# Kernel tuning notes

Measured on AMD Instinct MI355X. Metric: run time of the kernel, lower is better.

## Reference

```python
import jax, jax.numpy as jnp
import numpy as np

VOCAB = 100000
NUM_SENSES = 8
VEC_DIM = 128
BATCH = 16384
CTX = 10  # context words -> x has 2 + CTX columns


def setup_inputs() -> dict:
    key = jax.random.key(0)
    kx, kg, ks = jax.random.split(key, 3)
    x = jax.random.randint(kx, (BATCH, 2 + CTX), 0, VOCAB, dtype=jnp.int32)
    W_g = jax.random.normal(kg, (VOCAB, VEC_DIM), dtype=jnp.float32) * 0.1
    W_s = jax.random.normal(ks, (VOCAB, NUM_SENSES, VEC_DIM), dtype=jnp.float32) * 0.1
    return {"x": x, "W_g": W_g, "W_s": W_s}


def reference(x, W_g, W_s):
    # sum of global vectors of the context words: [B, D]
    sum_context = jnp.sum(W_g[x[:, 2:]], axis=1)
    # sense vectors of the target word: [B, K, D]
    sense_vecs = W_s[x[:, 0]]
    # per-sense score against the context: [B, K]
    scores = jnp.einsum("bkd,bd->bk", sense_vecs, sum_context)
    # route to best sense per example: [B]
    right_senses = jnp.argmax(scores, axis=1)
    # gather the chosen sense vector: [B, D]
    chosen = jnp.take_along_axis(sense_vecs, right_senses[:, None, None], axis=1)[:, 0, :]
    # dot with the global vector of the second word -> [B, 1], sigmoid activation
    dot_prod = jnp.einsum("bd,bd->b", chosen, W_g[x[:, 1]])[:, None]
    return jax.nn.sigmoid(dot_prod)
```

## Files before the change

### kernel.cpp

```cpp
#include <hip/hip_runtime.h>
#include <hip/hip_bf16.h>
#include <cmath>

#define BATCH     16384
#define CTX       10
#define NSENSE    8
#define VEC_DIM   128
#define XCOLS     (2 + CTX)

__global__ __launch_bounds__(256) void SenseEmbedding_40295383171457_kernel(
    const int*   __restrict__ x,
    const float* __restrict__ Wg,
    const float* __restrict__ Ws,
    float*       __restrict__ out)
{
    const int gtid = blockIdx.x * blockDim.x + threadIdx.x;
    const int elem = gtid >> 4;
    const int sub  = gtid & 15;
    if (elem >= BATCH) return;

    const int* xr = x + elem * XCOLS;
    const int w0 = xr[0];
    const int w1 = xr[1];
    const int off = sub * 8;

    float4 c0 = make_float4(0.f, 0.f, 0.f, 0.f);
    float4 c1 = make_float4(0.f, 0.f, 0.f, 0.f);
    #pragma unroll
    for (int c = 0; c < CTX; ++c) {
        const float* row = Wg + (size_t)xr[2 + c] * VEC_DIM + off;
        const float4 a = *reinterpret_cast<const float4*>(row);
        const float4 b = *reinterpret_cast<const float4*>(row + 4);
        c0.x += a.x; c0.y += a.y; c0.z += a.z; c0.w += a.w;
        c1.x += b.x; c1.y += b.y; c1.z += b.z; c1.w += b.w;
    }

    const float* srow = Ws + (size_t)w0 * (NSENSE * VEC_DIM);
    float scores[NSENSE];
    #pragma unroll
    for (int k = 0; k < NSENSE; ++k) {
        const float* r = srow + k * VEC_DIM + off;
        const float4 a = *reinterpret_cast<const float4*>(r);
        const float4 b = *reinterpret_cast<const float4*>(r + 4);
        float p = a.x * c0.x + a.y * c0.y + a.z * c0.z + a.w * c0.w
                + b.x * c1.x + b.y * c1.y + b.z * c1.z + b.w * c1.w;
        #pragma unroll
        for (int s = 8; s > 0; s >>= 1)
            p += __shfl_xor(p, s, 16);
        scores[k] = p;
    }

    int   best = 0;
    float bv   = scores[0];
    #pragma unroll
    for (int k = 1; k < NSENSE; ++k) {
        if (scores[k] > bv) { bv = scores[k]; best = k; }
    }

    const float* ch = srow + best * VEC_DIM + off;
    const float4 ca = *reinterpret_cast<const float4*>(ch);
    const float4 cb = *reinterpret_cast<const float4*>(ch + 4);
    const float* tg = Wg + (size_t)w1 * VEC_DIM + off;
    const float4 ta = *reinterpret_cast<const float4*>(tg);
    const float4 tb = *reinterpret_cast<const float4*>(tg + 4);
    float d = ca.x * ta.x + ca.y * ta.y + ca.z * ta.z + ca.w * ta.w
            + cb.x * tb.x + cb.y * tb.y + cb.z * tb.z + cb.w * tb.w;
    #pragma unroll
    for (int s = 8; s > 0; s >>= 1)
        d += __shfl_xor(d, s, 16);

    if (sub == 0) {
        out[elem] = 1.f / (1.f + expf(-d));
    }
}

extern "C" void kernel_launch(void* const* d_in, const int* in_sizes, int n_in,
                              void* d_out, int out_size, void* d_ws, size_t ws_size,
                              hipStream_t stream) {
    const int*   x  = (const int*)  d_in[0];
    const float* Wg = (const float*)d_in[1];
    const float* Ws = (const float*)d_in[2];
    float*       out = (float*)d_out;

    const int elems_per_block = 256 / 16;
    const int grid = (BATCH + elems_per_block - 1) / elems_per_block;
    SenseEmbedding_40295383171457_kernel<<<grid, 256, 0, stream>>>(x, Wg, Ws, out);
}
```

Before: 489.2 us.

## Precompute target dots for all senses to drop dependent chosen-sense reload

Loads the x row as three int4 vectors and issues the target-word Wg load up front. While the sense rows are in registers, it computes the dot of each sense with the target vector, then selects the partial for the argmax sense instead of reloading the chosen row after the argmax. This removes a serialized, argmax-dependent global load and lets all memory loads issue early. In exchange it does extra FMAs, raises register use, and relies on 48-byte aligned x rows for the int4 loads.

```diff
diff --git a/kernel.cpp b/kernel.cpp
--- a/kernel.cpp
+++ b/kernel.cpp
@@ -19,58 +19,68 @@
     const int sub  = gtid & 15;
     if (elem >= BATCH) return;
 
-    const int* xr = x + elem * XCOLS;
-    const int w0 = xr[0];
-    const int w1 = xr[1];
+    const int4* xr4 = reinterpret_cast<const int4*>(x + elem * XCOLS);
+    const int4 xa = xr4[0];
+    const int4 xb = xr4[1];
+    const int4 xc = xr4[2];
     const int off = sub * 8;
 
+    const float* tgt = Wg + (size_t)xa.y * VEC_DIM + off;
+    const float4 t0 = *reinterpret_cast<const float4*>(tgt);
+    const float4 t1 = *reinterpret_cast<const float4*>(tgt + 4);
+
+    const int cidx[CTX] = {xa.z, xa.w, xb.x, xb.y, xb.z, xb.w,
+                           xc.x, xc.y, xc.z, xc.w};
     float4 c0 = make_float4(0.f, 0.f, 0.f, 0.f);
     float4 c1 = make_float4(0.f, 0.f, 0.f, 0.f);
     #pragma unroll
     for (int c = 0; c < CTX; ++c) {
-        const float* row = Wg + (size_t)xr[2 + c] * VEC_DIM + off;
+        const float* row = Wg + (size_t)cidx[c] * VEC_DIM + off;
         const float4 a = *reinterpret_cast<const float4*>(row);
         const float4 b = *reinterpret_cast<const float4*>(row + 4);
         c0.x += a.x; c0.y += a.y; c0.z += a.z; c0.w += a.w;
         c1.x += b.x; c1.y += b.y; c1.z += b.z; c1.w += b.w;
     }
 
-    const float* srow = Ws + (size_t)w0 * (NSENSE * VEC_DIM);
-    float scores[NSENSE];
+    const float* srow = Ws + (size_t)xa.x * (NSENSE * VEC_DIM);
+    float p[NSENSE], q[NSENSE];
     #pragma unroll
     for (int k = 0; k < NSENSE; ++k) {
         const float* r = srow + k * VEC_DIM + off;
         const float4 a = *reinterpret_cast<const float4*>(r);
         const float4 b = *reinterpret_cast<const float4*>(r + 4);
-        float p = a.x * c0.x + a.y * c0.y + a.z * c0.z + a.w * c0.w
-                + b.x * c1.x + b.y * c1.y + b.z * c1.z + b.w * c1.w;
+        p[k] = a.x * c0.x + a.y * c0.y + a.z * c0.z + a.w * c0.w
+             + b.x * c1.x + b.y * c1.y + b.z * c1.z + b.w * c1.w;
+        q[k] = a.x * t0.x + a.y * t0.y + a.z * t0.z + a.w * t0.w
+             + b.x * t1.x + b.y * t1.y + b.z * t1.z + b.w * t1.w;
+    }
+
+    #pragma unroll
+    for (int k = 0; k < NSENSE; ++k) {
+        float v = p[k];
         #pragma unroll
         for (int s = 8; s > 0; s >>= 1)
-            p += __shfl_xor(p, s, 16);
-        scores[k] = p;
+            v += __shfl_xor(v, s, 16);
+        p[k] = v;
     }
 
     int   best = 0;
-    float bv   = scores[0];
+    float bv   = p[0];
     #pragma unroll
     for (int k = 1; k < NSENSE; ++k) {
-        if (scores[k] > bv) { bv = scores[k]; best = k; }
+        if (p[k] > bv) { bv = p[k]; best = k; }
     }
 
-    const float* ch = srow + best * VEC_DIM + off;
-    const float4 ca = *reinterpret_cast<const float4*>(ch);
-    const float4 cb = *reinterpret_cast<const float4*>(ch + 4);
-    const float* tg = Wg + (size_t)w1 * VEC_DIM + off;
-    const float4 ta = *reinterpret_cast<const float4*>(tg);
-    const float4 tb = *reinterpret_cast<const float4*>(tg + 4);
-    float d = ca.x * ta.x + ca.y * ta.y + ca.z * ta.z + ca.w * ta.w
-            + cb.x * tb.x + cb.y * tb.y + cb.z * tb.z + cb.w * tb.w;
+    float qb = q[0];
+    #pragma unroll
+    for (int k = 1; k < NSENSE; ++k)
+        qb = (best == k) ? q[k] : qb;
     #pragma unroll
     for (int s = 8; s > 0; s >>= 1)
-        d += __shfl_xor(d, s, 16);
+        qb += __shfl_xor(qb, s, 16);
 
     if (sub == 0) {
-        out[elem] = 1.f / (1.f + expf(-d));
+        out[elem] = 1.f / (1.f + expf(-qb));
     }
 }
 
```

Result: no change. 483.9 us (-1.1%).
